# Optimization experiments

Hardware: AMD Instinct MI355X
Metric: run time of the kernel (lower is better)

## Reference

```python
import jax, jax.numpy as jnp
import numpy as np
import math

B, S, DIM, H, KVH = 2, 2048, 2048, 16, 4
HD = DIM // H          # 128
G = H // KVH           # 4 (GQA repeat factor)
NEG = -1e9             # fp32 additive mask value (matches torch path)


def _rotate_half(x):
    x1, x2 = jnp.split(x, 2, axis=-1)
    return jnp.concatenate([-x2, x1], axis=-1)


def setup_inputs() -> dict:
    key = jax.random.key(0)
    ks = jax.random.split(key, 8)
    hidden_states = jax.random.normal(ks[0], (B, S, DIM), jnp.float32)
    # standard RoPE tables [S, HD]
    inv_freq = 1.0 / (10000.0 ** (jnp.arange(0, HD, 2, dtype=jnp.float32) / HD))
    freqs = jnp.outer(jnp.arange(S, dtype=jnp.float32), inv_freq)
    emb = jnp.concatenate([freqs, freqs], axis=-1)
    position_cos = jnp.cos(emb)
    position_sin = jnp.sin(emb)
    alibi_bias = jax.random.normal(ks[1], (B, S, S), jnp.float32) * 0.01
    attention_mask = jnp.zeros((B, 1, 1, S), jnp.float32)
    sc = 0.02
    wq = jax.random.normal(ks[2], (DIM, DIM), jnp.float32) * sc
    wk = jax.random.normal(ks[3], (DIM, KVH * HD), jnp.float32) * sc
    wv = jax.random.normal(ks[4], (DIM, KVH * HD), jnp.float32) * sc
    wo = jax.random.normal(ks[5], (DIM, DIM), jnp.float32) * sc
    return {"hidden_states": hidden_states, "position_cos": position_cos,
            "position_sin": position_sin, "alibi_bias": alibi_bias,
            "attention_mask": attention_mask, "wq": wq, "wk": wk, "wv": wv, "wo": wo}


def reference(hidden_states, position_cos, position_sin, alibi_bias,
              attention_mask, wq, wk, wv, wo):
    b, s, d = hidden_states.shape
    # projections (weights stored as [in, out])
    q = (hidden_states @ wq).reshape(b, s, H, HD).transpose(0, 2, 1, 3)      # [B,H,S,HD]
    k = (hidden_states @ wk).reshape(b, s, KVH, HD).transpose(0, 2, 1, 3)    # [B,KVH,S,HD]
    v = (hidden_states @ wv).reshape(b, s, KVH, HD).transpose(0, 2, 1, 3)
    # RoPE
    cos = position_cos[None, None]  # [1,1,S,HD]
    sin = position_sin[None, None]
    q = q * cos + _rotate_half(q) * sin
    k = k * cos + _rotate_half(k) * sin
    # GQA repeat kv heads
    k = jnp.repeat(k, G, axis=1)   # [B,H,S,HD]
    v = jnp.repeat(v, G, axis=1)
    scores = jnp.einsum('bhqd,bhkd->bhqk', q, k) * (1.0 / math.sqrt(HD))
    causal = jnp.triu(jnp.full((s, s), NEG, jnp.float32), 1)
    scores = scores + causal + alibi_bias[:, None, :, :] + attention_mask
    attn = jax.nn.softmax(scores.astype(jnp.float32), axis=-1).astype(q.dtype)
    out = jnp.einsum('bhqk,bhkd->bhqd', attn, v)                              # [B,H,S,HD]
    out = out.transpose(0, 2, 1, 3).reshape(b, s, d)
    return out @ wo
```

## Files before the change

### kernel.cpp

```cpp
#include <hip/hip_runtime.h>
#include <hip/hip_bf16.h>

#define Bb   2
#define Ss   2048
#define Dd   2048
#define Hh   16
#define KVHh 4
#define HDd  128
#define QKVW 3072

typedef __bf16 bf16x8 __attribute__((ext_vector_type(8)));
typedef float f32x4 __attribute__((ext_vector_type(4)));

__device__ __forceinline__ unsigned short f2bf(float f) {
    unsigned u = __float_as_uint(f);
    unsigned r = (u + 0x7FFFu + ((u >> 16) & 1u)) >> 16;
    return (unsigned short)r;
}
__device__ __forceinline__ float bfu2f(unsigned short u) {
    return __uint_as_float(((unsigned)u) << 16);
}

#define GLOAD16(g, l) __builtin_amdgcn_global_load_lds( \
    (const __attribute__((address_space(1))) unsigned int*)(g), \
    (__attribute__((address_space(3))) unsigned int*)(l), 16, 0, 0)

__global__ __launch_bounds__(256)
void cast_bf16(const float* __restrict__ X, unsigned short* __restrict__ Y)
{
    int idx = blockIdx.x * 256 + threadIdx.x;
    float4 v = reinterpret_cast<const float4*>(X)[idx];
    ushort4 o;
    o.x = f2bf(v.x); o.y = f2bf(v.y); o.z = f2bf(v.z); o.w = f2bf(v.w);
    reinterpret_cast<ushort4*>(Y)[idx] = o;
}

__global__ __launch_bounds__(256)
void wt_cast_all(const float* __restrict__ wq, const float* __restrict__ wk,
                 const float* __restrict__ wv, const float* __restrict__ wo,
                 unsigned short* __restrict__ wqkvT, unsigned short* __restrict__ woT)
{
    __shared__ float tile[32][33];
    int id = blockIdx.x;
    const float* W; unsigned short* WT; int N, kx, ny;
    if (id < 4096)      {            W = wq; WT = wqkvT;                        N = 2048; kx = id & 63; ny = id >> 6; }
    else if (id < 5120) { id -= 4096; W = wk; WT = wqkvT + (size_t)2048 * 2048; N = 512;  kx = id & 63; ny = id >> 6; }
    else if (id < 6144) { id -= 5120; W = wv; WT = wqkvT + (size_t)2560 * 2048; N = 512;  kx = id & 63; ny = id >> 6; }
    else                { id -= 6144; W = wo; WT = woT;                         N = 2048; kx = id & 63; ny = id >> 6; }
    const int K = 2048;
    int k0 = kx * 32, n0 = ny * 32;
    int tx = threadIdx.x & 31, ty = threadIdx.x >> 5;
    #pragma unroll
    for (int i = 0; i < 32; i += 8)
        tile[ty + i][tx] = W[(size_t)(k0 + ty + i) * N + n0 + tx];
    __syncthreads();
    #pragma unroll
    for (int i = 0; i < 32; i += 8)
        WT[(size_t)(n0 + ty + i) * K + k0 + tx] = f2bf(tile[tx][ty + i]);
}

template<bool BF16OUT>
__global__ __launch_bounds__(256)
void gemm_bt(const unsigned short* __restrict__ A,
             const unsigned short* __restrict__ BT,
             void* __restrict__ Cv, int M, int N, int K)
{
    __shared__ __align__(16) unsigned short sA[128 * 32];
    __shared__ __align__(16) unsigned short sB[128 * 32];
    const int tid  = threadIdx.x;
    const int wave = tid >> 6;
    const int lane = tid & 63;
    const int m    = lane & 15;
    const int quad = lane >> 4;
    const int wm   = wave >> 1, wn = wave & 1;
    const int m0   = blockIdx.y * 128, n0 = blockIdx.x * 128;

    const int srow = tid >> 2;
    const int skg  = (tid & 3) * 8;

    f32x4 acc[4][4];
    #pragma unroll
    for (int r = 0; r < 4; ++r)
        #pragma unroll
        for (int c = 0; c < 4; ++c) acc[r][c] = (f32x4){0.f, 0.f, 0.f, 0.f};

    const unsigned short* pa = A  + (size_t)(m0 + srow) * K + skg;
    const unsigned short* pb = BT + (size_t)(n0 + srow) * K + skg;
    unsigned short* la = &sA[wave * 16 * 32];
    unsigned short* lb = &sB[wave * 16 * 32];

    for (int k0 = 0; k0 < K; k0 += 32) {
        GLOAD16(pa + k0, la);
        GLOAD16(pa + (size_t)64 * K + k0, la + 64 * 32);
        GLOAD16(pb + k0, lb);
        GLOAD16(pb + (size_t)64 * K + k0, lb + 64 * 32);
        __syncthreads();
        bf16x8 af[4], bfr[4];
        #pragma unroll
        for (int r = 0; r < 4; ++r)
            af[r] = *reinterpret_cast<const bf16x8*>(
                &sA[(wm * 64 + r * 16 + m) * 32 + quad * 8]);
        #pragma unroll
        for (int c = 0; c < 4; ++c)
            bfr[c] = *reinterpret_cast<const bf16x8*>(
                &sB[(wn * 64 + c * 16 + m) * 32 + quad * 8]);
        #pragma unroll
        for (int r = 0; r < 4; ++r)
            #pragma unroll
            for (int c = 0; c < 4; ++c)
                acc[r][c] = __builtin_amdgcn_mfma_f32_16x16x32_bf16(
                    af[r], bfr[c], acc[r][c], 0, 0, 0);
        __syncthreads();
    }
    #pragma unroll
    for (int r = 0; r < 4; ++r)
        #pragma unroll
        for (int c = 0; c < 4; ++c)
            #pragma unroll
            for (int e = 0; e < 4; ++e) {
                size_t row = m0 + wm * 64 + r * 16 + quad * 4 + e;
                size_t col = n0 + wn * 64 + c * 16 + m;
                if (BF16OUT)
                    ((unsigned short*)Cv)[row * N + col] = f2bf(acc[r][c][e]);
                else
                    ((float*)Cv)[row * N + col] = acc[r][c][e];
            }
}

__global__ __launch_bounds__(256)
void rope_all(unsigned short* __restrict__ qkv, const float* __restrict__ cosT,
              const float* __restrict__ sinT)
{
    const int h   = blockIdx.y;
    const int row = blockIdx.x * 4 + (threadIdx.x >> 6);
    const int i   = threadIdx.x & 63;
    const int s   = row & (Ss - 1);
    const float scale = (h < Hh) ? 0.08838834764831845f : 1.0f;
    unsigned short* xp = qkv + (size_t)row * QKVW + h * HDd;
    float x1 = bfu2f(xp[i]);
    float x2 = bfu2f(xp[i + 64]);
    float c1 = cosT[s * HDd + i];
    float c2 = cosT[s * HDd + i + 64];
    float s1 = sinT[s * HDd + i];
    float s2 = sinT[s * HDd + i + 64];
    xp[i]      = f2bf((x1 * c1 - x2 * s1) * scale);
    xp[i + 64] = f2bf((x2 * c2 + x1 * s2) * scale);
}

__global__ __launch_bounds__(256)
void vt_cast_bf(const unsigned short* __restrict__ KV,
                unsigned short* __restrict__ VT)
{
    __shared__ unsigned short tile[32][34];
    int st = blockIdx.x * 32, dt = blockIdx.y * 32;
    int bk = blockIdx.z;
    int b = bk >> 2, kvh = bk & 3;
    int tx = threadIdx.x & 31, ty = threadIdx.x >> 5;
    #pragma unroll
    for (int i = 0; i < 32; i += 8)
        tile[ty + i][tx] = KV[(size_t)(b * Ss + st + ty + i) * QKVW + 2560 + kvh * HDd + dt + tx];
    __syncthreads();
    #pragma unroll
    for (int i = 0; i < 32; i += 8)
        VT[(((size_t)b * KVHh + kvh) * HDd + dt + ty + i) * Ss + st + tx] =
            tile[tx][ty + i];
}

__global__ __launch_bounds__(256, 2)
void flash_attn(const unsigned short* __restrict__ qkv,
                const unsigned short* __restrict__ VT,
                const float* __restrict__ alibi,
                const float* __restrict__ amask,
                unsigned short* __restrict__ ctx)
{
    __shared__ __align__(16) unsigned short kbuf[3][32 * 128];
    __shared__ __align__(16) unsigned short vbuf[3][128 * 32];
    __shared__ __align__(16) float          abuf[3][2][512];
    __shared__ __align__(16) float          am_lds[Ss];
    __shared__ unsigned short s_p[4][16][56];

    const int tid  = threadIdx.x;
    const int w    = tid >> 6;
    const int m    = tid & 15;
    const int quad = (tid & 63) >> 4;

    const int kvh = blockIdx.y;
    const int b   = blockIdx.z;
    const int h   = kvh * 4 + w;

    const int x    = blockIdx.x;
    const int qtA0 = (x & 1) ? (63 - (x >> 1)) : (x >> 1);
    const int qtA  = b ? (63 - qtA0) : qtA0;
    const int qtB  = 127 - qtA;
    const int qA0  = qtA * 16, qB0 = qtB * 16;
    const int ntA  = (qA0 + 47) >> 5;
    const int ntB  = (qB0 + 47) >> 5;

    const unsigned short* vt0 = VT + ((size_t)b * KVHh + kvh) * HDd * Ss;
    const float* amrow = amask + (size_t)b * Ss;
    const float* arowA = alibi + ((size_t)b * Ss + qA0) * Ss;
    const float* arowB = alibi + ((size_t)b * Ss + qB0) * Ss;
    const unsigned short* kgbase = qkv + (size_t)b * Ss * QKVW + 2048 + kvh * HDd;

    const int krow_s = tid >> 4;
    const int koff_b = ((tid & 15) * 16) ^ ((krow_s & 7) << 4);
    const int vrow_s = tid >> 2;
    const int vchk_s = (tid & 3) ^ ((vrow_s >> 1) & 3);
    const int dstw   = w * 512;

    {
        const float* ag = amrow + tid * 4;
        GLOAD16(ag,        am_lds + w * 256);
        GLOAD16(ag + 1024, am_lds + 1024 + w * 256);
    }
    bf16x8 qaA[4], qaB[4];
    {
        const unsigned short* qrA = qkv + (size_t)(b * Ss + qA0 + m) * QKVW + h * HDd;
        const unsigned short* qrB = qkv + (size_t)(b * Ss + qB0 + m) * QKVW + h * HDd;
        #pragma unroll
        for (int c = 0; c < 4; ++c) {
            qaA[c] = *reinterpret_cast<const bf16x8*>(qrA + c * 32 + quad * 8);
            qaB[c] = *reinterpret_cast<const bf16x8*>(qrB + c * 32 + quad * 8);
        }
    }

    f32x4 oA[8], oB[8];
    #pragma unroll
    for (int f = 0; f < 8; ++f) {
        oA[f] = (f32x4){0.f, 0.f, 0.f, 0.f};
        oB[f] = (f32x4){0.f, 0.f, 0.f, 0.f};
    }
    float lA[4] = {0.f, 0.f, 0.f, 0.f}, lB[4] = {0.f, 0.f, 0.f, 0.f};

    auto STAGE = [&](int kn, int buf, bool aact) {
        const unsigned short* kg =
            kgbase + (size_t)(kn + krow_s) * QKVW + (koff_b >> 1);
        GLOAD16(kg,              &kbuf[buf][dstw]);
        GLOAD16(kg + 16 * QKVW,  &kbuf[buf][2048 + dstw]);
        const unsigned short* vg = vt0 + (size_t)vrow_s * Ss + kn + vchk_s * 8;
        GLOAD16(vg,             &vbuf[buf][dstw]);
        GLOAD16(vg + 64 * Ss,   &vbuf[buf][2048 + dstw]);
        if (tid < 128) {
            if (aact) {
                const float* ag = arowA + (size_t)(tid >> 3) * Ss + kn + (tid & 7) * 4;
                GLOAD16(ag, &abuf[buf][0][w * 256]);
            }
        } else {
            const float* ag = arowB + (size_t)((tid - 128) >> 3) * Ss + kn + (tid & 7) * 4;
            GLOAD16(ag, &abuf[buf][1][(w - 2) * 256]);
        }
    };

    STAGE(0, 0, true);
    asm volatile("s_waitcnt vmcnt(0)" ::: "memory");
    __syncthreads();

    int cur = 0;
    #pragma unroll 1
    for (int kt = 0; kt < ntB; ++kt) {
        const int k0  = kt * 32;
        const int nxt = (cur == 2) ? 0 : cur + 1;
        const bool aact = kt < ntA;

        if (kt + 1 < ntB) {
            const bool aactn = (kt + 1) < ntA;
            STAGE(k0 + 32, nxt, aactn);
            if (w < 2) {
                if (aactn) asm volatile("s_waitcnt vmcnt(5)" ::: "memory");
                else       asm volatile("s_waitcnt vmcnt(4)" ::: "memory");
            } else       asm volatile("s_waitcnt vmcnt(5)" ::: "memory");
        } else {
            asm volatile("s_waitcnt vmcnt(0)" ::: "memory");
        }
        __builtin_amdgcn_s_barrier();
        __builtin_amdgcn_sched_barrier(0);

        const float am0 = am_lds[k0 + m];
        const float am1 = am_lds[k0 + 16 + m];

        const char* kb  = (const char*)&kbuf[cur][0];
        const char* vbp = (const char*)&vbuf[cur][0];
        const int  ksw  = (m & 7) << 4;
        const int  vsw  = ((m >> 1) & 3) << 4;
        bf16x8 kf0[4], kf1[4];
        #pragma unroll
        for (int c = 0; c < 4; ++c) {
            kf0[c] = *(const bf16x8*)(kb + m * 256        + ((c * 64 + quad * 16) ^ ksw));
            kf1[c] = *(const bf16x8*)(kb + (16 + m) * 256 + ((c * 64 + quad * 16) ^ ksw));
        }
        bf16x8 vf[8];
        #pragma unroll
        for (int f = 0; f < 8; ++f)
            vf[f] = *(const bf16x8*)(vbp + (f * 16 + m) * 64 + ((quad * 16) ^ vsw));

        {
            f32x4 s0 = {0.f, 0.f, 0.f, 0.f}, s1 = {0.f, 0.f, 0.f, 0.f};
            #pragma unroll
            for (int c = 0; c < 4; ++c) {
                s0 = __builtin_amdgcn_mfma_f32_16x16x32_bf16(qaB[c], kf0[c], s0, 0, 0, 0);
                s1 = __builtin_amdgcn_mfma_f32_16x16x32_bf16(qaB[c], kf1[c], s1, 0, 0, 0);
            }
            #pragma unroll
            for (int r = 0; r < 4; ++r) {
                const int row = quad * 4 + r;
                const int qi  = qB0 + row;
                float x0 = s0[r] + abuf[cur][1][row * 32 + m]      + am0;
                float x1 = s1[r] + abuf[cur][1][row * 32 + 16 + m] + am1;
                x0 = (k0 + m      <= qi) ? x0 : -1e30f;
                x1 = (k0 + 16 + m <= qi) ? x1 : -1e30f;
                const float p0 = __expf(x0);
                const float p1 = __expf(x1);
                lB[r] += p0 + p1;
                s_p[w][row][m]      = f2bf(p0);
                s_p[w][row][16 + m] = f2bf(p1);
            }
            __builtin_amdgcn_wave_barrier();
            const bf16x8 pa = *reinterpret_cast<const bf16x8*>(&s_p[w][m][quad * 8]);
            __builtin_amdgcn_wave_barrier();
            #pragma unroll
            for (int f = 0; f < 8; ++f)
                oB[f] = __builtin_amdgcn_mfma_f32_16x16x32_bf16(pa, vf[f], oB[f], 0, 0, 0);
        }

        if (aact) {
            f32x4 s0 = {0.f, 0.f, 0.f, 0.f}, s1 = {0.f, 0.f, 0.f, 0.f};
            #pragma unroll
            for (int c = 0; c < 4; ++c) {
                s0 = __builtin_amdgcn_mfma_f32_16x16x32_bf16(qaA[c], kf0[c], s0, 0, 0, 0);
                s1 = __builtin_amdgcn_mfma_f32_16x16x32_bf16(qaA[c], kf1[c], s1, 0, 0, 0);
            }
            #pragma unroll
            for (int r = 0; r < 4; ++r) {
                const int row = quad * 4 + r;
                const int qi  = qA0 + row;
                float x0 = s0[r] + abuf[cur][0][row * 32 + m]      + am0;
                float x1 = s1[r] + abuf[cur][0][row * 32 + 16 + m] + am1;
                x0 = (k0 + m      <= qi) ? x0 : -1e30f;
                x1 = (k0 + 16 + m <= qi) ? x1 : -1e30f;
                const float p0 = __expf(x0);
                const float p1 = __expf(x1);
                lA[r] += p0 + p1;
                s_p[w][row][m]      = f2bf(p0);
                s_p[w][row][16 + m] = f2bf(p1);
            }
            __builtin_amdgcn_wave_barrier();
            const bf16x8 pa = *reinterpret_cast<const bf16x8*>(&s_p[w][m][quad * 8]);
            __builtin_amdgcn_wave_barrier();
            #pragma unroll
            for (int f = 0; f < 8; ++f)
                oA[f] = __builtin_amdgcn_mfma_f32_16x16x32_bf16(pa, vf[f], oA[f], 0, 0, 0);
        }

        cur = nxt;
    }

    float invA[4], invB[4];
    #pragma unroll
    for (int r = 0; r < 4; ++r) {
        float la = lA[r], lb = lB[r];
        la += __shfl_xor(la, 1, 64); lb += __shfl_xor(lb, 1, 64);
        la += __shfl_xor(la, 2, 64); lb += __shfl_xor(lb, 2, 64);
        la += __shfl_xor(la, 4, 64); lb += __shfl_xor(lb, 4, 64);
        la += __shfl_xor(la, 8, 64); lb += __shfl_xor(lb, 8, 64);
        invA[r] = 1.f / la; invB[r] = 1.f / lb;
    }
    #pragma unroll
    for (int f = 0; f < 8; ++f)
        #pragma unroll
        for (int r = 0; r < 4; ++r) {
            ctx[(size_t)(b * Ss + qA0 + quad * 4 + r) * Dd + h * HDd + f * 16 + m] =
                f2bf(oA[f][r] * invA[r]);
            ctx[(size_t)(b * Ss + qB0 + quad * 4 + r) * Dd + h * HDd + f * 16 + m] =
                f2bf(oB[f][r] * invB[r]);
        }
}

extern "C" void kernel_launch(void* const* d_in, const int* in_sizes, int n_in,
                              void* d_out, int out_size, void* d_ws, size_t ws_size,
                              hipStream_t stream) {
    const float* hidden = (const float*)d_in[0];
    const float* cosT   = (const float*)d_in[1];
    const float* sinT   = (const float*)d_in[2];
    const float* alibi  = (const float*)d_in[3];
    const float* amask  = (const float*)d_in[4];
    const float* wq     = (const float*)d_in[5];
    const float* wk     = (const float*)d_in[6];
    const float* wv     = (const float*)d_in[7];
    const float* wo     = (const float*)d_in[8];
    float* out = (float*)d_out;

    char* ws = (char*)d_ws;
    unsigned short* Abf    = (unsigned short*)(ws);
    unsigned short* wqkvT  = (unsigned short*)(ws + 16777216);
    unsigned short* woT    = (unsigned short*)(ws + 29360128);
    unsigned short* QKVraw = (unsigned short*)(ws + 37748736);
    unsigned short* VT     = (unsigned short*)(ws + 62914560);
    unsigned short* Ctx    = (unsigned short*)(ws + 67108864);

    const int M = Bb * Ss;

    cast_bf16<<<(M * Dd / 4) / 256, 256, 0, stream>>>(hidden, Abf);
    wt_cast_all<<<10240, 256, 0, stream>>>(wq, wk, wv, wo, wqkvT, woT);

    gemm_bt<true><<<dim3(QKVW / 128, M / 128), 256, 0, stream>>>(Abf, wqkvT, QKVraw, M, QKVW, Dd);

    rope_all<<<dim3(M / 4, 20), 256, 0, stream>>>(QKVraw, cosT, sinT);

    vt_cast_bf<<<dim3(Ss / 32, HDd / 32, Bb * KVHh), 256, 0, stream>>>(QKVraw, VT);

    flash_attn<<<dim3(64, KVHh, Bb), 256, 0, stream>>>(QKVraw, VT, alibi, amask, Ctx);

    gemm_bt<false><<<dim3(Dd / 128, M / 128), 256, 0, stream>>>(Ctx, woT, out, M, Dd, Dd);
}
```

Measured before the change: 363.2 us.

## Replace GEMM with 256x256-tile, 8-wave, 4-buffer pipelined bf16 MFMA kernel

```diff
diff --git a/kernel.cpp b/kernel.cpp
--- a/kernel.cpp
+++ b/kernel.cpp
@@ -60,70 +60,109 @@
 }
 
 template<bool BF16OUT>
-__global__ __launch_bounds__(256)
-void gemm_bt(const unsigned short* __restrict__ A,
+__global__ __launch_bounds__(512, 2)
+void gemm256(const unsigned short* __restrict__ A,
              const unsigned short* __restrict__ BT,
              void* __restrict__ Cv, int M, int N, int K)
 {
-    __shared__ __align__(16) unsigned short sA[128 * 32];
-    __shared__ __align__(16) unsigned short sB[128 * 32];
+    __shared__ __align__(16) unsigned short sA[4][256 * 32];
+    __shared__ __align__(16) unsigned short sB[4][256 * 32];
     const int tid  = threadIdx.x;
-    const int wave = tid >> 6;
+    const int w    = tid >> 6;
     const int lane = tid & 63;
     const int m    = lane & 15;
     const int quad = lane >> 4;
-    const int wm   = wave >> 1, wn = wave & 1;
-    const int m0   = blockIdx.y * 128, n0 = blockIdx.x * 128;
+    const int wm   = w >> 2;
+    const int wn   = w & 3;
+    const int m0   = blockIdx.y * 256, n0 = blockIdx.x * 256;
 
     const int srow = tid >> 2;
-    const int skg  = (tid & 3) * 8;
-
-    f32x4 acc[4][4];
-    #pragma unroll
-    for (int r = 0; r < 4; ++r)
-        #pragma unroll
-        for (int c = 0; c < 4; ++c) acc[r][c] = (f32x4){0.f, 0.f, 0.f, 0.f};
-
-    const unsigned short* pa = A  + (size_t)(m0 + srow) * K + skg;
-    const unsigned short* pb = BT + (size_t)(n0 + srow) * K + skg;
-    unsigned short* la = &sA[wave * 16 * 32];
-    unsigned short* lb = &sB[wave * 16 * 32];
-
-    for (int k0 = 0; k0 < K; k0 += 32) {
-        GLOAD16(pa + k0, la);
-        GLOAD16(pa + (size_t)64 * K + k0, la + 64 * 32);
-        GLOAD16(pb + k0, lb);
-        GLOAD16(pb + (size_t)64 * K + k0, lb + 64 * 32);
-        __syncthreads();
-        bf16x8 af[4], bfr[4];
-        #pragma unroll
-        for (int r = 0; r < 4; ++r)
-            af[r] = *reinterpret_cast<const bf16x8*>(
-                &sA[(wm * 64 + r * 16 + m) * 32 + quad * 8]);
-        #pragma unroll
-        for (int c = 0; c < 4; ++c)
-            bfr[c] = *reinterpret_cast<const bf16x8*>(
-                &sB[(wn * 64 + c * 16 + m) * 32 + quad * 8]);
-        #pragma unroll
-        for (int r = 0; r < 4; ++r)
-            #pragma unroll
-            for (int c = 0; c < 4; ++c)
-                acc[r][c] = __builtin_amdgcn_mfma_f32_16x16x32_bf16(
-                    af[r], bfr[c], acc[r][c], 0, 0, 0);
-        __syncthreads();
-    }
-    #pragma unroll
-    for (int r = 0; r < 4; ++r)
-        #pragma unroll
-        for (int c = 0; c < 4; ++c)
+    const int scol = (tid & 3) ^ (((tid >> 5) & 1) << 1);
+    const int chk  = quad ^ (((m >> 3) & 1) << 1);
+
+    f32x4 acc[8][4];
+    #pragma unroll
+    for (int fm = 0; fm < 8; ++fm)
+        #pragma unroll
+        for (int fn = 0; fn < 4; ++fn) acc[fm][fn] = (f32x4){0.f, 0.f, 0.f, 0.f};
+
+    auto STAGE2 = [&](int T, int h) {
+        const int buf = T & 3;
+        GLOAD16(A  + (size_t)(m0 + h * 128 + srow) * K + T * 32 + scol * 8,
+                (char*)sA + buf * 16384 + h * 8192 + w * 1024);
+        GLOAD16(BT + (size_t)(n0 + h * 128 + srow) * K + T * 32 + scol * 8,
+                (char*)sB + buf * 16384 + h * 8192 + w * 1024);
+    };
+
+    const int NT = K >> 5;
+
+    STAGE2(0, 0); STAGE2(0, 1); STAGE2(1, 0); STAGE2(1, 1);
+    asm volatile("s_waitcnt vmcnt(4)" ::: "memory");
+    __builtin_amdgcn_s_barrier();
+    __builtin_amdgcn_sched_barrier(0);
+
+    #pragma unroll 1
+    for (int t = 0; t < NT; ++t) {
+        const int buf = t & 3;
+        const char* ab = (const char*)sA + buf * 16384 + wm * 8192;
+        const char* bb = (const char*)sB + buf * 16384 + (wn >> 1) * 8192 + (wn & 1) * 4096;
+
+        bf16x8 bf[4], af[4];
+        #pragma unroll
+        for (int fn = 0; fn < 4; ++fn)
+            bf[fn] = *(const bf16x8*)(bb + (fn * 16 + m) * 64 + chk * 16);
+        #pragma unroll
+        for (int j = 0; j < 4; ++j)
+            af[j] = *(const bf16x8*)(ab + (j * 16 + m) * 64 + chk * 16);
+        if (t + 2 < NT) STAGE2(t + 2, 0);
+        __builtin_amdgcn_sched_barrier(0);
+        __builtin_amdgcn_s_barrier();
+        __builtin_amdgcn_sched_barrier(0);
+        __builtin_amdgcn_s_setprio(1);
+        #pragma unroll
+        for (int j = 0; j < 4; ++j)
+            #pragma unroll
+            for (int fn = 0; fn < 4; ++fn)
+                acc[j][fn] = __builtin_amdgcn_mfma_f32_16x16x32_bf16(
+                    af[j], bf[fn], acc[j][fn], 0, 0, 0);
+        __builtin_amdgcn_s_setprio(0);
+        __builtin_amdgcn_s_barrier();
+        __builtin_amdgcn_sched_barrier(0);
+
+        #pragma unroll
+        for (int j = 0; j < 4; ++j)
+            af[j] = *(const bf16x8*)(ab + ((4 + j) * 16 + m) * 64 + chk * 16);
+        if (t + 2 < NT) STAGE2(t + 2, 1);
+        __builtin_amdgcn_sched_barrier(0);
+        __builtin_amdgcn_s_barrier();
+        __builtin_amdgcn_sched_barrier(0);
+        __builtin_amdgcn_s_setprio(1);
+        #pragma unroll
+        for (int j = 0; j < 4; ++j)
+            #pragma unroll
+            for (int fn = 0; fn < 4; ++fn)
+                acc[4 + j][fn] = __builtin_amdgcn_mfma_f32_16x16x32_bf16(
+                    af[j], bf[fn], acc[4 + j][fn], 0, 0, 0);
+        __builtin_amdgcn_s_setprio(0);
+
+        if (t + 2 < NT)      asm volatile("s_waitcnt vmcnt(4)" ::: "memory");
+        else if (t + 1 < NT) asm volatile("s_waitcnt vmcnt(0)" ::: "memory");
+        __builtin_amdgcn_s_barrier();
+        __builtin_amdgcn_sched_barrier(0);
+    }
+
+    #pragma unroll
+    for (int fm = 0; fm < 8; ++fm)
+        #pragma unroll
+        for (int fn = 0; fn < 4; ++fn)
             #pragma unroll
             for (int e = 0; e < 4; ++e) {
-                size_t row = m0 + wm * 64 + r * 16 + quad * 4 + e;
-                size_t col = n0 + wn * 64 + c * 16 + m;
+                size_t row = m0 + wm * 128 + fm * 16 + quad * 4 + e;
+                size_t col = n0 + wn * 64 + fn * 16 + m;
                 if (BF16OUT)
-                    ((unsigned short*)Cv)[row * N + col] = f2bf(acc[r][c][e]);
+                    ((unsigned short*)Cv)[row * N + col] = f2bf(acc[fm][fn][e]);
                 else
-                    ((float*)Cv)[row * N + col] = acc[r][c][e];
+                    ((float*)Cv)[row * N + col] = acc[fm][fn][e];
             }
 }
 
@@ -402,7 +441,7 @@
     cast_bf16<<<(M * Dd / 4) / 256, 256, 0, stream>>>(hidden, Abf);
     wt_cast_all<<<10240, 256, 0, stream>>>(wq, wk, wv, wo, wqkvT, woT);
 
-    gemm_bt<true><<<dim3(QKVW / 128, M / 128), 256, 0, stream>>>(Abf, wqkvT, QKVraw, M, QKVW, Dd);
+    gemm256<true><<<dim3(QKVW / 256, M / 256), 512, 0, stream>>>(Abf, wqkvT, QKVraw, M, QKVW, Dd);
 
     rope_all<<<dim3(M / 4, 20), 256, 0, stream>>>(QKVraw, cosT, sinT);
 
@@ -410,5 +449,5 @@
 
     flash_attn<<<dim3(64, KVHh, Bb), 256, 0, stream>>>(QKVraw, VT, alibi, amask, Ctx);
 
-    gemm_bt<false><<<dim3(Dd / 128, M / 128), 256, 0, stream>>>(Ctx, woT, out, M, Dd, Dd);
-}
+    gemm256<false><<<dim3(Dd / 256, M / 256), 512, 0, stream>>>(Ctx, woT, out, M, Dd, Dd);
+}
```

New measurement: 363.6 us. About the same (+0.1%).
